# Kernel tuning notes

Hardware: AMD Instinct MI355X
Metric: run time of the kernel (lower is better)

The kernel has to match this reference:

```python
import jax, jax.numpy as jnp
import numpy as np

B, S, H = 4096, 256, 64


def setup_inputs() -> dict:
    key = jax.random.key(0)
    ks = jax.random.split(key, 9)
    s = 1.0 / np.sqrt(H)
    return {
        "x": jax.random.normal(ks[0], (B, S), jnp.float32),
        "W1": jax.random.normal(ks[1], (4, 1), jnp.float32),
        "b1": jax.random.normal(ks[2], (4,), jnp.float32) * 0.1,
        "W_ih": jax.random.normal(ks[3], (4 * H, 4), jnp.float32) * s,
        "W_hh": jax.random.normal(ks[4], (4 * H, H), jnp.float32) * s,
        "b_ih": jax.random.normal(ks[5], (4 * H,), jnp.float32) * s,
        "b_hh": jax.random.normal(ks[6], (4 * H,), jnp.float32) * s,
        "W2": jax.random.normal(ks[7], (1, H), jnp.float32) * s,
        "b2": jax.random.normal(ks[8], (1,), jnp.float32) * 0.1,
    }


def _lstm_last_h(fc1, W_ih, W_hh, b_ih, b_hh):
    # fc1: (B, S, 4). Precompute input contribution to gates for all steps.
    gx = jnp.einsum('bsi,gi->sbg', fc1, W_ih) + (b_ih + b_hh)  # (S, B, 4H)
    h0 = jnp.zeros((fc1.shape[0], H), fc1.dtype)
    c0 = jnp.zeros_like(h0)

    def step(carry, g_t):
        h, c = carry
        gates = g_t + h @ W_hh.T  # (B, 4H)
        i, f, g, o = jnp.split(gates, 4, axis=-1)  # PyTorch gate order i,f,g,o
        i = jax.nn.sigmoid(i)
        f = jax.nn.sigmoid(f)
        g = jnp.tanh(g)
        o = jax.nn.sigmoid(o)
        c = f * c + i * g
        h = o * jnp.tanh(c)
        return (h, c), None

    (h_last, _), _ = jax.lax.scan(step, (h0, c0), gx)
    return h_last  # (B, H)


def reference(x, W1, b1, W_ih, W_hh, b_ih, b_hh, W2, b2):
    # fc1: Linear(1->4) + tanh on x.unsqueeze(2)
    fc1 = jnp.tanh(x[..., None] * W1[:, 0] + b1)  # (B, S, 4)
    h_last = _lstm_last_h(fc1, W_ih, W_hh, b_ih, b_hh)
    return h_last @ W2.T + b2  # (B, 1)
```

## Files before the change

kernel.cpp:

```cpp
#include <hip/hip_runtime.h>


typedef __attribute__((ext_vector_type(8))) __bf16 bf16x8;
typedef __attribute__((ext_vector_type(4))) float f32x4;

#define S_LEN 256
#define HID 64
#define TB 16
#define CHUNK 64
#define LOG2E 1.4426950408889634f

#if defined(__has_builtin) && __has_builtin(__builtin_amdgcn_exp2f)
#define EXP2F(x) __builtin_amdgcn_exp2f(x)
#else
#define EXP2F(x) exp2f(x)
#endif
#if defined(__has_builtin) && __has_builtin(__builtin_amdgcn_rcpf)
#define RCPF(x) __builtin_amdgcn_rcpf(x)
#else
#define RCPF(x) (1.0f / (x))
#endif

__device__ __forceinline__ float fast_sigmoid(float x) {
    float e = EXP2F(-LOG2E * x);
    return RCPF(1.0f + e);
}
__device__ __forceinline__ float fast_tanh(float x) {
    float e = EXP2F(2.0f * LOG2E * x);
    return 1.0f - 2.0f * RCPF(e + 1.0f);
}

__global__ __launch_bounds__(256, 1)
void lstm_fused(const float* __restrict__ x,
                const float* __restrict__ W1, const float* __restrict__ b1,
                const float* __restrict__ W_ih, const float* __restrict__ W_hh,
                const float* __restrict__ b_ih, const float* __restrict__ b_hh,
                const float* __restrict__ W2, const float* __restrict__ b2,
                float* __restrict__ out)
{
    __shared__ float fc1c[CHUNK][TB][4];
    __shared__ __bf16 hbuf[2][2][2][4][TB][8];
    __shared__ float hfin[HID][TB];

    const int tid  = threadIdx.x;
    const int lane = tid & 63;
    const int wv   = tid >> 6;
    const int col  = lane & 15;
    const int kg   = lane >> 4;
    const int b0   = blockIdx.x * TB;

    bf16x8 whh_h[4][2], whh_l[4][2];
    float  wihv[4][4];
    float  biasv[4];
    #pragma unroll
    for (int n = 0; n < 4; ++n) {
        const int g = 16 * (wv + 4 * n) + col;
        #pragma unroll
        for (int ks = 0; ks < 2; ++ks) {
            const float* wp = &W_hh[g * 64 + ks * 32 + kg * 8];
            #pragma unroll
            for (int j = 0; j < 8; ++j) {
                float wf  = wp[j];
                __bf16 hi = (__bf16)wf;
                whh_h[n][ks][j] = hi;
                whh_l[n][ks][j] = (__bf16)(wf - (float)hi);
            }
        }
        #pragma unroll
        for (int j = 0; j < 4; ++j) wihv[n][j] = W_ih[g * 4 + j];
        biasv[n] = b_ih[g] + b_hh[g];
    }

    {
        __bf16* p = &hbuf[0][0][0][0][0][0];
        #pragma unroll
        for (int j = 0; j < 8; ++j) p[tid * 8 + j] = (__bf16)0.0f;
    }

    float w1r[4], b1r[4];
    #pragma unroll
    for (int j = 0; j < 4; ++j) { w1r[j] = W1[j]; b1r[j] = b1[j]; }

    f32x4 cst = {0.f, 0.f, 0.f, 0.f};
    float hlast[4];

    const int u   = 16 * wv + col;
    const int uks = u >> 5, ukg = (u >> 3) & 3, up = u & 7;

    for (int t = 0; t < S_LEN; ++t) {
        if ((t & (CHUNK - 1)) == 0) {
            __syncthreads();
            const int rr = tid & 15;
            const int tq = tid >> 4;
            f32x4 xv = *(const f32x4*)&x[(b0 + rr) * S_LEN + t + tq * 4];
            #pragma unroll
            for (int tl = 0; tl < 4; ++tl) {
                #pragma unroll
                for (int j = 0; j < 4; ++j)
                    fc1c[tq * 4 + tl][rr][j] = fast_tanh(xv[tl] * w1r[j] + b1r[j]);
            }
            __syncthreads();
        }
        const int cur = t & 1, nxt = cur ^ 1;

        bf16x8 ah0 = *(const bf16x8*)&hbuf[cur][0][0][kg][col][0];
        bf16x8 ah1 = *(const bf16x8*)&hbuf[cur][0][1][kg][col][0];
        bf16x8 al0 = *(const bf16x8*)&hbuf[cur][1][0][kg][col][0];
        bf16x8 al1 = *(const bf16x8*)&hbuf[cur][1][1][kg][col][0];

        f32x4 acc[4];
        #pragma unroll
        for (int n = 0; n < 4; ++n) {
            f32x4 a = {0.f, 0.f, 0.f, 0.f};
            a = __builtin_amdgcn_mfma_f32_16x16x32_bf16(ah0, whh_h[n][0], a, 0, 0, 0);
            a = __builtin_amdgcn_mfma_f32_16x16x32_bf16(ah1, whh_h[n][1], a, 0, 0, 0);
            a = __builtin_amdgcn_mfma_f32_16x16x32_bf16(al0, whh_h[n][0], a, 0, 0, 0);
            a = __builtin_amdgcn_mfma_f32_16x16x32_bf16(al1, whh_h[n][1], a, 0, 0, 0);
            a = __builtin_amdgcn_mfma_f32_16x16x32_bf16(ah0, whh_l[n][0], a, 0, 0, 0);
            a = __builtin_amdgcn_mfma_f32_16x16x32_bf16(ah1, whh_l[n][1], a, 0, 0, 0);
            acc[n] = a;
        }

        float gxv[4][4];
        #pragma unroll
        for (int r = 0; r < 4; ++r) {
            f32x4 fv = *(const f32x4*)&fc1c[t & (CHUNK - 1)][kg * 4 + r][0];
            #pragma unroll
            for (int n = 0; n < 4; ++n) {
                float s = biasv[n];
                s = fmaf(fv[0], wihv[n][0], s);
                s = fmaf(fv[1], wihv[n][1], s);
                s = fmaf(fv[2], wihv[n][2], s);
                s = fmaf(fv[3], wihv[n][3], s);
                gxv[n][r] = s;
            }
        }

        #pragma unroll
        for (int r = 0; r < 4; ++r) {
            float iv = fast_sigmoid(acc[0][r] + gxv[0][r]);
            float fg = fast_sigmoid(acc[1][r] + gxv[1][r]);
            float gv = fast_tanh   (acc[2][r] + gxv[2][r]);
            float ov = fast_sigmoid(acc[3][r] + gxv[3][r]);
            float cv = fg * cst[r] + iv * gv;
            cst[r] = cv;
            float hv = ov * fast_tanh(cv);
            hlast[r] = hv;
            __bf16 hi = (__bf16)hv;
            __bf16 lo = (__bf16)(hv - (float)hi);
            const int rw = kg * 4 + r;
            hbuf[nxt][0][uks][ukg][rw][up] = hi;
            hbuf[nxt][1][uks][ukg][rw][up] = lo;
        }
        __syncthreads();
    }

    #pragma unroll
    for (int r = 0; r < 4; ++r) hfin[u][kg * 4 + r] = hlast[r];
    __syncthreads();
    if (tid < TB) {
        float s = b2[0];
        #pragma unroll
        for (int uu = 0; uu < HID; ++uu) s += hfin[uu][tid] * W2[uu];
        out[b0 + tid] = s;
    }
}

extern "C" void kernel_launch(void* const* d_in, const int* in_sizes, int n_in,
                              void* d_out, int out_size, void* d_ws, size_t ws_size,
                              hipStream_t stream) {
    (void)in_sizes; (void)n_in; (void)d_ws; (void)ws_size; (void)out_size;
    const float* x    = (const float*)d_in[0];
    const float* W1   = (const float*)d_in[1];
    const float* b1   = (const float*)d_in[2];
    const float* W_ih = (const float*)d_in[3];
    const float* W_hh = (const float*)d_in[4];
    const float* b_ih = (const float*)d_in[5];
    const float* b_hh = (const float*)d_in[6];
    const float* W2   = (const float*)d_in[7];
    const float* b2   = (const float*)d_in[8];
    float* out = (float*)d_out;
    lstm_fused<<<256, 256, 0, stream>>>(x, W1, b1, W_ih, W_hh, b_ih, b_hh, W2, b2, out);
}
```

Before: 257.7 us.

## Halve batch rows per block and split MFMA accumulation chains

Cuts each block's batch tile from 16 to 8 rows, which doubles the grid to 512 blocks, and allows 2 blocks per CU. The MFMA tile still covers 16 rows, so half its rows are padding (zero h). Lanes exchange accumulator halves with a shuffle so each lane evaluates the gates for only 2 rows instead of 4. The three MFMA dependency chains per gate are now independent and summed at the end, which shortens the serial MFMA latency. The cost is half-wasted MFMA work and higher register pressure under the 2-blocks-per-CU launch bound.

```diff
diff --git a/kernel.cpp b/kernel.cpp
--- a/kernel.cpp
+++ b/kernel.cpp
@@ -3,10 +3,11 @@
 
 typedef __attribute__((ext_vector_type(8))) __bf16 bf16x8;
 typedef __attribute__((ext_vector_type(4))) float f32x4;
+typedef __attribute__((ext_vector_type(2))) float f32x2;
 
 #define S_LEN 256
 #define HID 64
-#define TB 16
+#define TB 8
 #define CHUNK 64
 #define LOG2E 1.4426950408889634f
 
@@ -30,7 +31,7 @@
     return 1.0f - 2.0f * RCPF(e + 1.0f);
 }
 
-__global__ __launch_bounds__(256, 1)
+__global__ __launch_bounds__(256, 2)
 void lstm_fused(const float* __restrict__ x,
                 const float* __restrict__ W1, const float* __restrict__ b1,
                 const float* __restrict__ W_ih, const float* __restrict__ W_hh,
@@ -39,7 +40,7 @@
                 float* __restrict__ out)
 {
     __shared__ float fc1c[CHUNK][TB][4];
-    __shared__ __bf16 hbuf[2][2][2][4][TB][8];
+    __shared__ __bf16 hbuf[2][2][2][4][16][8];
     __shared__ float hfin[HID][TB];
 
     const int tid  = threadIdx.x;
@@ -72,17 +73,20 @@
     }
 
     {
-        __bf16* p = &hbuf[0][0][0][0][0][0];
-        #pragma unroll
-        for (int j = 0; j < 8; ++j) p[tid * 8 + j] = (__bf16)0.0f;
+        f32x4* z = (f32x4*)&hbuf[0][0][0][0][0][0];
+        f32x4 zv = {0.f, 0.f, 0.f, 0.f};
+        z[tid] = zv; z[tid + 256] = zv;
     }
 
     float w1r[4], b1r[4];
     #pragma unroll
     for (int j = 0; j < 4; ++j) { w1r[j] = W1[j]; b1r[j] = b1[j]; }
 
-    f32x4 cst = {0.f, 0.f, 0.f, 0.f};
-    float hlast[4];
+    const int row_base = (kg & 1) * 4 + (kg >> 1) * 2;
+    const bool upper   = (kg >= 2);
+
+    f32x2 cst = {0.f, 0.f};
+    float hlast[2];
 
     const int u   = 16 * wv + col;
     const int uks = u >> 5, ukg = (u >> 3) & 3, up = u & 7;
@@ -90,14 +94,14 @@
     for (int t = 0; t < S_LEN; ++t) {
         if ((t & (CHUNK - 1)) == 0) {
             __syncthreads();
-            const int rr = tid & 15;
-            const int tq = tid >> 4;
-            f32x4 xv = *(const f32x4*)&x[(b0 + rr) * S_LEN + t + tq * 4];
+            const int rr = tid & 7;
+            const int tq = tid >> 3;
+            f32x2 xv = *(const f32x2*)&x[(b0 + rr) * S_LEN + t + tq * 2];
             #pragma unroll
-            for (int tl = 0; tl < 4; ++tl) {
+            for (int tl = 0; tl < 2; ++tl) {
                 #pragma unroll
                 for (int j = 0; j < 4; ++j)
-                    fc1c[tq * 4 + tl][rr][j] = fast_tanh(xv[tl] * w1r[j] + b1r[j]);
+                    fc1c[tq * 2 + tl][rr][j] = fast_tanh(xv[tl] * w1r[j] + b1r[j]);
             }
             __syncthreads();
         }
@@ -108,23 +112,24 @@
         bf16x8 al0 = *(const bf16x8*)&hbuf[cur][1][0][kg][col][0];
         bf16x8 al1 = *(const bf16x8*)&hbuf[cur][1][1][kg][col][0];
 
-        f32x4 acc[4];
+        f32x4 accS[4];
         #pragma unroll
         for (int n = 0; n < 4; ++n) {
-            f32x4 a = {0.f, 0.f, 0.f, 0.f};
-            a = __builtin_amdgcn_mfma_f32_16x16x32_bf16(ah0, whh_h[n][0], a, 0, 0, 0);
-            a = __builtin_amdgcn_mfma_f32_16x16x32_bf16(ah1, whh_h[n][1], a, 0, 0, 0);
-            a = __builtin_amdgcn_mfma_f32_16x16x32_bf16(al0, whh_h[n][0], a, 0, 0, 0);
-            a = __builtin_amdgcn_mfma_f32_16x16x32_bf16(al1, whh_h[n][1], a, 0, 0, 0);
-            a = __builtin_amdgcn_mfma_f32_16x16x32_bf16(ah0, whh_l[n][0], a, 0, 0, 0);
-            a = __builtin_amdgcn_mfma_f32_16x16x32_bf16(ah1, whh_l[n][1], a, 0, 0, 0);
-            acc[n] = a;
+            f32x4 z4 = {0.f, 0.f, 0.f, 0.f};
+            f32x4 a = __builtin_amdgcn_mfma_f32_16x16x32_bf16(ah0, whh_h[n][0], z4, 0, 0, 0);
+            a       = __builtin_amdgcn_mfma_f32_16x16x32_bf16(ah1, whh_h[n][1], a,  0, 0, 0);
+            f32x4 b = __builtin_amdgcn_mfma_f32_16x16x32_bf16(al0, whh_h[n][0], z4, 0, 0, 0);
+            b       = __builtin_amdgcn_mfma_f32_16x16x32_bf16(al1, whh_h[n][1], b,  0, 0, 0);
+            f32x4 c = __builtin_amdgcn_mfma_f32_16x16x32_bf16(ah0, whh_l[n][0], z4, 0, 0, 0);
+            c       = __builtin_amdgcn_mfma_f32_16x16x32_bf16(ah1, whh_l[n][1], c,  0, 0, 0);
+            accS[n] = (a + b) + c;
         }
 
-        float gxv[4][4];
+        const int tloc = t & (CHUNK - 1);
+        float gxv[4][2];
         #pragma unroll
-        for (int r = 0; r < 4; ++r) {
-            f32x4 fv = *(const f32x4*)&fc1c[t & (CHUNK - 1)][kg * 4 + r][0];
+        for (int r = 0; r < 2; ++r) {
+            f32x4 fv = *(const f32x4*)&fc1c[tloc][row_base + r][0];
             #pragma unroll
             for (int n = 0; n < 4; ++n) {
                 float s = biasv[n];
@@ -136,19 +141,28 @@
             }
         }
 
+        float gsel[4][2];
         #pragma unroll
-        for (int r = 0; r < 4; ++r) {
-            float iv = fast_sigmoid(acc[0][r] + gxv[0][r]);
-            float fg = fast_sigmoid(acc[1][r] + gxv[1][r]);
-            float gv = fast_tanh   (acc[2][r] + gxv[2][r]);
-            float ov = fast_sigmoid(acc[3][r] + gxv[3][r]);
+        for (int n = 0; n < 4; ++n) {
+            float s2 = __shfl_xor(accS[n][2], 32);
+            float s3 = __shfl_xor(accS[n][3], 32);
+            gsel[n][0] = upper ? s2 : accS[n][0];
+            gsel[n][1] = upper ? s3 : accS[n][1];
+        }
+
+        #pragma unroll
+        for (int r = 0; r < 2; ++r) {
+            float iv = fast_sigmoid(gsel[0][r] + gxv[0][r]);
+            float fg = fast_sigmoid(gsel[1][r] + gxv[1][r]);
+            float gv = fast_tanh   (gsel[2][r] + gxv[2][r]);
+            float ov = fast_sigmoid(gsel[3][r] + gxv[3][r]);
             float cv = fg * cst[r] + iv * gv;
             cst[r] = cv;
             float hv = ov * fast_tanh(cv);
             hlast[r] = hv;
             __bf16 hi = (__bf16)hv;
             __bf16 lo = (__bf16)(hv - (float)hi);
-            const int rw = kg * 4 + r;
+            const int rw = row_base + r;
             hbuf[nxt][0][uks][ukg][rw][up] = hi;
             hbuf[nxt][1][uks][ukg][rw][up] = lo;
         }
@@ -156,7 +170,7 @@
     }
 
     #pragma unroll
-    for (int r = 0; r < 4; ++r) hfin[u][kg * 4 + r] = hlast[r];
+    for (int r = 0; r < 2; ++r) hfin[u][row_base + r] = hlast[r];
     __syncthreads();
     if (tid < TB) {
         float s = b2[0];
@@ -180,5 +194,5 @@
     const float* W2   = (const float*)d_in[7];
     const float* b2   = (const float*)d_in[8];
     float* out = (float*)d_out;
-    lstm_fused<<<256, 256, 0, stream>>>(x, W1, b1, W_ih, W_hh, b_ih, b_hh, W2, b2, out);
+    lstm_fused<<<4096 / TB, 256, 0, stream>>>(x, W1, b1, W_ih, W_hh, b_ih, b_hh, W2, b2, out);
 }
```

After: 311.0 us. 1.21x slower.

## Fold input projection and bias into MFMA, prescale gates by log2e, unroll steps

Applied to the files above, without the earlier changes.

The per-step input-to-gate projection (fc1 times W_ih plus bias) now runs as an extra MFMA on the tensor cores. It uses a hi/lo bf16 split of fc1 and W_ih and seeds the accumulator with the bias, replacing the scalar FMA loop. W_hh, W_ih and the biases are prescaled by log2(e), or 2·log2(e) for the g gate, so the activations call exp2 directly without a multiply. The time loop is unrolled by two with fixed double-buffer indices. This trades VALU work for one more MFMA per gate on the serial recurrence path.

```diff
diff --git a/kernel.cpp b/kernel.cpp
--- a/kernel.cpp
+++ b/kernel.cpp
@@ -5,7 +5,6 @@
 typedef __attribute__((ext_vector_type(4))) float f32x4;
 
 #define S_LEN 256
-#define HID 64
 #define TB 16
 #define CHUNK 64
 #define LOG2E 1.4426950408889634f
@@ -21,14 +20,49 @@
 #define RCPF(x) (1.0f / (x))
 #endif
 
-__device__ __forceinline__ float fast_sigmoid(float x) {
-    float e = EXP2F(-LOG2E * x);
-    return RCPF(1.0f + e);
-}
 __device__ __forceinline__ float fast_tanh(float x) {
     float e = EXP2F(2.0f * LOG2E * x);
     return 1.0f - 2.0f * RCPF(e + 1.0f);
 }
+
+#define MFMA16(A, B, C) __builtin_amdgcn_mfma_f32_16x16x32_bf16((A), (B), (C), 0, 0, 0)
+
+#define STEP(RB, WB, TLOC) do {                                                   \
+    bf16x8 ah0 = *(const bf16x8*)&hbuf[RB][0][0][kg][col][0];                     \
+    bf16x8 ah1 = *(const bf16x8*)&hbuf[RB][0][1][kg][col][0];                     \
+    bf16x8 al0 = *(const bf16x8*)&hbuf[RB][1][0][kg][col][0];                     \
+    bf16x8 al1 = *(const bf16x8*)&hbuf[RB][1][1][kg][col][0];                     \
+    bf16x8 fa  = *(const bf16x8*)&fcfrag[TLOC][col][0];                           \
+    if (kg >= 2) fa = zero8;                                                      \
+    f32x4 acc[4];                                                                 \
+    _Pragma("unroll")                                                             \
+    for (int n = 0; n < 4; ++n) {                                                 \
+        f32x4 a = MFMA16(fa,  whx[n],      biasq[n]);      \
+        a       = MFMA16(ah0, whh_h[n][0], a);                                    \
+        a       = MFMA16(ah1, whh_h[n][1], a);                                    \
+        a       = MFMA16(al0, whh_h[n][0], a);                                    \
+        a       = MFMA16(al1, whh_h[n][1], a);                                    \
+        a       = MFMA16(ah0, whh_l[n][0], a);                                    \
+        a       = MFMA16(ah1, whh_l[n][1], a);                                    \
+        acc[n] = a;                                                               \
+    }                                                                             \
+    _Pragma("unroll")                                                             \
+    for (int r = 0; r < 4; ++r) {                                                 \
+                        \
+        float ei = EXP2F(-acc[0][r]); float iv = RCPF(1.0f + ei);                 \
+        float ef = EXP2F(-acc[1][r]); float fv = RCPF(1.0f + ef);                 \
+        float eg = EXP2F( acc[2][r]); float gv = 1.0f - 2.0f * RCPF(1.0f + eg);   \
+        float eo = EXP2F(-acc[3][r]); float ov = RCPF(1.0f + eo);                 \
+        float cv = fv * cst[r] + iv * gv; cst[r] = cv;                            \
+        float ec = EXP2F((2.0f * LOG2E) * cv);                                    \
+        float th = 1.0f - 2.0f * RCPF(1.0f + ec);                                 \
+        float hv = ov * th; hlast[r] = hv;                                        \
+        __bf16 hi = (__bf16)hv; __bf16 lo = (__bf16)(hv - (float)hi);             \
+        hbuf[WB][0][uks][ukg][kg * 4 + r][up] = hi;                               \
+        hbuf[WB][1][uks][ukg][kg * 4 + r][up] = lo;                               \
+    }                                                                             \
+    __syncthreads();                                                              \
+} while (0)
 
 __global__ __launch_bounds__(256, 1)
 void lstm_fused(const float* __restrict__ x,
@@ -38,9 +72,9 @@
                 const float* __restrict__ W2, const float* __restrict__ b2,
                 float* __restrict__ out)
 {
-    __shared__ float fc1c[CHUNK][TB][4];
+    __shared__ __bf16 fcfrag[CHUNK][TB][8];
     __shared__ __bf16 hbuf[2][2][2][4][TB][8];
-    __shared__ float hfin[HID][TB];
+    __shared__ float hfin[64][TB];
 
     const int tid  = threadIdx.x;
     const int lane = tid & 63;
@@ -50,44 +84,58 @@
     const int b0   = blockIdx.x * TB;
 
     bf16x8 whh_h[4][2], whh_l[4][2];
-    float  wihv[4][4];
-    float  biasv[4];
+    bf16x8 whx[4];
+    f32x4  biasq[4];
+
+    bf16x8 zero8;
+    #pragma unroll
+    for (int j = 0; j < 8; ++j) zero8[j] = (__bf16)0.0f;
+
     #pragma unroll
     for (int n = 0; n < 4; ++n) {
         const int g = 16 * (wv + 4 * n) + col;
+        const float sc = (n == 2) ? (2.0f * LOG2E) : LOG2E;
         #pragma unroll
         for (int ks = 0; ks < 2; ++ks) {
             const float* wp = &W_hh[g * 64 + ks * 32 + kg * 8];
             #pragma unroll
             for (int j = 0; j < 8; ++j) {
-                float wf  = wp[j];
+                float wf  = sc * wp[j];
                 __bf16 hi = (__bf16)wf;
                 whh_h[n][ks][j] = hi;
                 whh_l[n][ks][j] = (__bf16)(wf - (float)hi);
             }
         }
-        #pragma unroll
-        for (int j = 0; j < 4; ++j) wihv[n][j] = W_ih[g * 4 + j];
-        biasv[n] = b_ih[g] + b_hh[g];
+        whx[n] = zero8;
+        if (kg < 2) {
+            #pragma unroll
+            for (int j = 0; j < 4; ++j) {
+                float wf  = sc * W_ih[g * 4 + j];
+                __bf16 hi = (__bf16)wf;
+                __bf16 v  = (kg == 0) ? hi : (__bf16)(wf - (float)hi);
+                whx[n][j] = v; whx[n][j + 4] = v;
+            }
+        }
+        const float bs = sc * (b_ih[g] + b_hh[g]);
+        biasq[n][0] = bs; biasq[n][1] = bs; biasq[n][2] = bs; biasq[n][3] = bs;
     }
 
     {
-        __bf16* p = &hbuf[0][0][0][0][0][0];
-        #pragma unroll
-        for (int j = 0; j < 8; ++j) p[tid * 8 + j] = (__bf16)0.0f;
+        f32x4 zv = {0.f, 0.f, 0.f, 0.f};
+        ((f32x4*)&hbuf[0][0][0][0][0][0])[tid] = zv;
     }
 
     float w1r[4], b1r[4];
     #pragma unroll
     for (int j = 0; j < 4; ++j) { w1r[j] = W1[j]; b1r[j] = b1[j]; }
 
-    f32x4 cst = {0.f, 0.f, 0.f, 0.f};
+    float cst[4] = {0.f, 0.f, 0.f, 0.f};
     float hlast[4];
 
     const int u   = 16 * wv + col;
     const int uks = u >> 5, ukg = (u >> 3) & 3, up = u & 7;
 
-    for (int t = 0; t < S_LEN; ++t) {
+    for (int t = 0; t < S_LEN; t += 2) {
         if ((t & (CHUNK - 1)) == 0) {
             __syncthreads();
             const int rr = tid & 15;
@@ -95,64 +143,20 @@
             f32x4 xv = *(const f32x4*)&x[(b0 + rr) * S_LEN + t + tq * 4];
             #pragma unroll
             for (int tl = 0; tl < 4; ++tl) {
+                bf16x8 v;
                 #pragma unroll
-                for (int j = 0; j < 4; ++j)
-                    fc1c[tq * 4 + tl][rr][j] = fast_tanh(xv[tl] * w1r[j] + b1r[j]);
+                for (int j = 0; j < 4; ++j) {
+                    float fc  = fast_tanh(xv[tl] * w1r[j] + b1r[j]);
+                    __bf16 hi = (__bf16)fc;
+                    v[j]     = hi;
+                    v[j + 4] = (__bf16)(fc - (float)hi);
+                }
+                *(bf16x8*)&fcfrag[tq * 4 + tl][rr][0] = v;
             }
             __syncthreads();
         }
-        const int cur = t & 1, nxt = cur ^ 1;
-
-        bf16x8 ah0 = *(const bf16x8*)&hbuf[cur][0][0][kg][col][0];
-        bf16x8 ah1 = *(const bf16x8*)&hbuf[cur][0][1][kg][col][0];
-        bf16x8 al0 = *(const bf16x8*)&hbuf[cur][1][0][kg][col][0];
-        bf16x8 al1 = *(const bf16x8*)&hbuf[cur][1][1][kg][col][0];
-
-        f32x4 acc[4];
-        #pragma unroll
-        for (int n = 0; n < 4; ++n) {
-            f32x4 a = {0.f, 0.f, 0.f, 0.f};
-            a = __builtin_amdgcn_mfma_f32_16x16x32_bf16(ah0, whh_h[n][0], a, 0, 0, 0);
-            a = __builtin_amdgcn_mfma_f32_16x16x32_bf16(ah1, whh_h[n][1], a, 0, 0, 0);
-            a = __builtin_amdgcn_mfma_f32_16x16x32_bf16(al0, whh_h[n][0], a, 0, 0, 0);
-            a = __builtin_amdgcn_mfma_f32_16x16x32_bf16(al1, whh_h[n][1], a, 0, 0, 0);
-            a = __builtin_amdgcn_mfma_f32_16x16x32_bf16(ah0, whh_l[n][0], a, 0, 0, 0);
-            a = __builtin_amdgcn_mfma_f32_16x16x32_bf16(ah1, whh_l[n][1], a, 0, 0, 0);
-            acc[n] = a;
-        }
-
-        float gxv[4][4];
-        #pragma unroll
-        for (int r = 0; r < 4; ++r) {
-            f32x4 fv = *(const f32x4*)&fc1c[t & (CHUNK - 1)][kg * 4 + r][0];
-            #pragma unroll
-            for (int n = 0; n < 4; ++n) {
-                float s = biasv[n];
-                s = fmaf(fv[0], wihv[n][0], s);
-                s = fmaf(fv[1], wihv[n][1], s);
-                s = fmaf(fv[2], wihv[n][2], s);
-                s = fmaf(fv[3], wihv[n][3], s);
-                gxv[n][r] = s;
-            }
-        }
-
-        #pragma unroll
-        for (int r = 0; r < 4; ++r) {
-            float iv = fast_sigmoid(acc[0][r] + gxv[0][r]);
-            float fg = fast_sigmoid(acc[1][r] + gxv[1][r]);
-            float gv = fast_tanh   (acc[2][r] + gxv[2][r]);
-            float ov = fast_sigmoid(acc[3][r] + gxv[3][r]);
-            float cv = fg * cst[r] + iv * gv;
-            cst[r] = cv;
-            float hv = ov * fast_tanh(cv);
-            hlast[r] = hv;
-            __bf16 hi = (__bf16)hv;
-            __bf16 lo = (__bf16)(hv - (float)hi);
-            const int rw = kg * 4 + r;
-            hbuf[nxt][0][uks][ukg][rw][up] = hi;
-            hbuf[nxt][1][uks][ukg][rw][up] = lo;
-        }
-        __syncthreads();
+        STEP(0, 1, (t & (CHUNK - 1)));
+        STEP(1, 0, ((t + 1) & (CHUNK - 1)));
     }
 
     #pragma unroll
@@ -161,7 +165,7 @@
     if (tid < TB) {
         float s = b2[0];
         #pragma unroll
-        for (int uu = 0; uu < HID; ++uu) s += hfin[uu][tid] * W2[uu];
+        for (int uu = 0; uu < 64; ++uu) s += hfin[uu][tid] * W2[uu];
         out[b0 + tid] = s;
     }
 }
@@ -180,5 +184,5 @@
     const float* W2   = (const float*)d_in[7];
     const float* b2   = (const float*)d_in[8];
     float* out = (float*)d_out;
-    lstm_fused<<<256, 256, 0, stream>>>(x, W1, b1, W_ih, W_hh, b_ih, b_hh, W2, b2, out);
+    lstm_fused<<<4096 / TB, 256, 0, stream>>>(x, W1, b1, W_ih, W_hh, b_ih, b_hh, W2, b2, out);
 }
```

Result: faster. 230.5 us (-10.5%).
